# Performance work log

Hardware: AMD Instinct MI355X
Metric: run time of the kernel (lower is better)

Reference implementation:

```python
import jax, jax.numpy as jnp
import numpy as np

LAMDA = 1.0


def setup_inputs() -> dict:
    key = jax.random.key(0)
    k1, k2, k3, k4 = jax.random.split(key, 4)
    B, C, D = 16384, 1000, 512
    logits = jax.random.normal(k1, (B, C), dtype=jnp.float32)
    labels = jax.random.randint(k2, (B,), 0, C, dtype=jnp.int64)
    features = jax.random.normal(k3, (B, D), dtype=jnp.float32)
    global_protos = jax.random.normal(k4, (C, D), dtype=jnp.float32)
    return {"logits": logits, "labels": labels, "features": features,
            "global_protos": global_protos}


def reference(logits, labels, features, global_protos):
    # --- classification loss: mean cross-entropy ---
    logp = jax.nn.log_softmax(logits, axis=-1)                 # [B, C]
    ce_loss = -jnp.take_along_axis(logp, labels[:, None], axis=1).mean()
    ce_loss = jnp.where(jnp.isfinite(ce_loss), ce_loss, 0.0)

    # --- prototype alignment loss ---
    # Every label has a (finite) global prototype, so the per-sample dict
    # loop reduces to: gather proto by label, per-sample MSE, mean over B.
    gathered = global_protos[labels]                           # [B, D]
    per_sample_mse = jnp.mean((features - gathered) ** 2, axis=-1)  # [B]
    proto_loss = per_sample_mse.mean()

    total_loss = ce_loss + LAMDA * proto_loss
    total_loss = jnp.where(jnp.isfinite(total_loss), total_loss, ce_loss)
    return (total_loss, ce_loss, proto_loss)
```

## Files before the change

kernel.cpp:

```cpp
#include <hip/hip_runtime.h>
#include <math.h>


#ifndef INFINITY
#define INFINITY __builtin_inff()
#endif

#define NB_MAX 2048

__global__ __launch_bounds__(256) void fedtgp_rows(
    const float* __restrict__ logits,
    const int*   __restrict__ labels,
    const float* __restrict__ features,
    const float* __restrict__ protos,
    double* __restrict__ ce_part,
    double* __restrict__ pl_part,
    int B, int C, int D)
{
    const int tid  = threadIdx.x;
    const int lane = tid & 63;
    const int wv   = tid >> 6;

    __shared__ float rmax[4];
    __shared__ float rsum[4];
    __shared__ float rsq[4];

    const int C4 = C >> 2;
    const int D4 = D >> 2;

    double ce_acc = 0.0;
    double pl_acc = 0.0;

    for (int row = blockIdx.x; row < B; row += gridDim.x) {
        const int lab = labels[row];
        const float4* lrow4 = (const float4*)(logits + (size_t)row * C);

        float4 lv = make_float4(0.f, 0.f, 0.f, 0.f);
        float m = -INFINITY;
        if (tid < C4) {
            lv = lrow4[tid];
            m = fmaxf(fmaxf(lv.x, lv.y), fmaxf(lv.z, lv.w));
        }
        #pragma unroll
        for (int off = 32; off > 0; off >>= 1)
            m = fmaxf(m, __shfl_xor(m, off, 64));
        if (lane == 0) rmax[wv] = m;
        __syncthreads();
        const float bmax = fmaxf(fmaxf(rmax[0], rmax[1]), fmaxf(rmax[2], rmax[3]));

        float s = 0.f;
        if (tid < C4) {
            s = __expf(lv.x - bmax) + __expf(lv.y - bmax)
              + __expf(lv.z - bmax) + __expf(lv.w - bmax);
        }
        #pragma unroll
        for (int off = 32; off > 0; off >>= 1)
            s += __shfl_xor(s, off, 64);
        if (lane == 0) rsum[wv] = s;

        float q = 0.f;
        if (tid < D4) {
            const float4 f = ((const float4*)(features + (size_t)row * D))[tid];
            const float4 p = ((const float4*)(protos   + (size_t)lab * D))[tid];
            const float dx = f.x - p.x, dy = f.y - p.y;
            const float dz = f.z - p.z, dw = f.w - p.w;
            q = dx*dx + dy*dy + dz*dz + dw*dw;
        }
        #pragma unroll
        for (int off = 32; off > 0; off >>= 1)
            q += __shfl_xor(q, off, 64);
        if (lane == 0) rsq[wv] = q;
        __syncthreads();

        if (tid == 0) {
            const float bsum = rsum[0] + rsum[1] + rsum[2] + rsum[3];
            const float bsq  = rsq[0]  + rsq[1]  + rsq[2]  + rsq[3];
            const float lse  = bmax + __logf(bsum);
            const float ce_b = lse - logits[(size_t)row * C + lab];
            ce_acc += (double)ce_b;
            pl_acc += (double)(bsq / (float)D);
        }
    }

    if (tid == 0) {
        ce_part[blockIdx.x] = ce_acc;
        pl_part[blockIdx.x] = pl_acc;
    }
}

__global__ __launch_bounds__(256) void fedtgp_finalize(
    const double* __restrict__ ce_part,
    const double* __restrict__ pl_part,
    float* __restrict__ out,
    int npart, double invB)
{
    const int tid  = threadIdx.x;
    const int lane = tid & 63;
    const int wv   = tid >> 6;
    __shared__ double rc[4];
    __shared__ double rp[4];

    double c = 0.0, p = 0.0;
    for (int i = tid; i < npart; i += 256) {
        c += ce_part[i];
        p += pl_part[i];
    }
    #pragma unroll
    for (int off = 32; off > 0; off >>= 1) {
        c += __shfl_xor(c, off, 64);
        p += __shfl_xor(p, off, 64);
    }
    if (lane == 0) { rc[wv] = c; rp[wv] = p; }
    __syncthreads();

    if (tid == 0) {
        const double cs = rc[0] + rc[1] + rc[2] + rc[3];
        const double ps = rp[0] + rp[1] + rp[2] + rp[3];
        float ce = (float)(cs * invB);
        float pl = (float)(ps * invB);
        if (!isfinite(ce)) ce = 0.0f;
        float tot = ce + pl;
        if (!isfinite(tot)) tot = ce;
        out[0] = tot;
        out[1] = ce;
        out[2] = pl;
    }
}

extern "C" void kernel_launch(void* const* d_in, const int* in_sizes, int n_in,
                              void* d_out, int out_size, void* d_ws, size_t ws_size,
                              hipStream_t stream)
{
    const float* logits   = (const float*)d_in[0];
    const int*   labels   = (const int*)  d_in[1];
    const float* features = (const float*)d_in[2];
    const float* protos   = (const float*)d_in[3];
    float* out = (float*)d_out;

    const int B = in_sizes[1];
    const int C = in_sizes[0] / B;
    const int D = in_sizes[2] / B;

    int nb = NB_MAX;
    const size_t need_per_block = 2 * sizeof(double);
    if ((size_t)nb * need_per_block > ws_size) {
        nb = (int)(ws_size / need_per_block);
        if (nb < 1) nb = 1;
    }
    if (nb > B) nb = B;

    double* ce_part = (double*)d_ws;
    double* pl_part = ce_part + nb;

    fedtgp_rows<<<nb, 256, 0, stream>>>(logits, labels, features, protos,
                                        ce_part, pl_part, B, C, D);
    fedtgp_finalize<<<1, 256, 0, stream>>>(ce_part, pl_part, out, nb, 1.0 / (double)B);
}
```

Before: 124.3 us.

## Process one row per wavefront with online softmax and shuffle-only reductions

Each row is now handled by a single 64-lane wavefront rather than a 256-thread block. Each lane computes an online max/sum-exp over strided float4 chunks, and the per-lane partials are merged with a shuffle butterfly. This removes the two __syncthreads and the shared-memory round trips per row, and also handles C or D values that are not multiples of 4. In exchange each wave issues more serial loads per row with fewer lanes active (250 float4 per 64 lanes), and the clamp of nb to B was removed.

New measurement: 121.6 us. -2.2%, faster.

```diff
diff --git a/kernel.cpp b/kernel.cpp
--- a/kernel.cpp
+++ b/kernel.cpp
@@ -6,7 +6,7 @@
 #define INFINITY __builtin_inff()
 #endif
 
-#define NB_MAX 2048
+#define NB 2048
 
 __global__ __launch_bounds__(256) void fedtgp_rows(
     const float* __restrict__ logits,
@@ -20,71 +20,91 @@
     const int tid  = threadIdx.x;
     const int lane = tid & 63;
     const int wv   = tid >> 6;
+    const int gw     = blockIdx.x * 4 + wv;
+    const int nwaves = gridDim.x * 4;
 
-    __shared__ float rmax[4];
-    __shared__ float rsum[4];
-    __shared__ float rsq[4];
+    const int C4   = C >> 2;
+    const int Crem = C & 3;
+    const int D4   = D >> 2;
+    const int Drem = D & 3;
 
-    const int C4 = C >> 2;
-    const int D4 = D >> 2;
+    double ce_acc = 0.0, pl_acc = 0.0;
 
-    double ce_acc = 0.0;
-    double pl_acc = 0.0;
+    for (int row = gw; row < B; row += nwaves) {
+        const float*  lrow = logits + (size_t)row * C;
+        const float4* l4   = (const float4*)lrow;
+        const int lab = labels[row];
+        const float ll = lrow[lab];
 
-    for (int row = blockIdx.x; row < B; row += gridDim.x) {
-        const int lab = labels[row];
-        const float4* lrow4 = (const float4*)(logits + (size_t)row * C);
+        float m = -INFINITY, s = 0.f;
+        for (int base = 0; base < C4; base += 256) {
+            float4 v[4];
+            #pragma unroll
+            for (int k = 0; k < 4; ++k) {
+                const int idx = base + lane + 64 * k;
+                v[k] = (idx < C4) ? l4[idx]
+                                  : make_float4(-INFINITY, -INFINITY, -INFINITY, -INFINITY);
+            }
+            float cm = m;
+            #pragma unroll
+            for (int k = 0; k < 4; ++k)
+                cm = fmaxf(cm, fmaxf(fmaxf(v[k].x, v[k].y), fmaxf(v[k].z, v[k].w)));
+            if (cm > -INFINITY) {
+                s *= __expf(m - cm);
+                #pragma unroll
+                for (int k = 0; k < 4; ++k) {
+                    s += __expf(v[k].x - cm) + __expf(v[k].y - cm)
+                       + __expf(v[k].z - cm) + __expf(v[k].w - cm);
+                }
+                m = cm;
+            }
+        }
+        if (Crem && lane < Crem) {
+            const float x = lrow[(C4 << 2) + lane];
+            const float cm = fmaxf(m, x);
+            s = s * __expf(m - cm) + __expf(x - cm);
+            m = cm;
+        }
 
-        float4 lv = make_float4(0.f, 0.f, 0.f, 0.f);
-        float m = -INFINITY;
-        if (tid < C4) {
-            lv = lrow4[tid];
-            m = fmaxf(fmaxf(lv.x, lv.y), fmaxf(lv.z, lv.w));
-        }
-        #pragma unroll
-        for (int off = 32; off > 0; off >>= 1)
-            m = fmaxf(m, __shfl_xor(m, off, 64));
-        if (lane == 0) rmax[wv] = m;
-        __syncthreads();
-        const float bmax = fmaxf(fmaxf(rmax[0], rmax[1]), fmaxf(rmax[2], rmax[3]));
-
-        float s = 0.f;
-        if (tid < C4) {
-            s = __expf(lv.x - bmax) + __expf(lv.y - bmax)
-              + __expf(lv.z - bmax) + __expf(lv.w - bmax);
-        }
-        #pragma unroll
-        for (int off = 32; off > 0; off >>= 1)
-            s += __shfl_xor(s, off, 64);
-        if (lane == 0) rsum[wv] = s;
-
+        const float4* f4 = (const float4*)(features + (size_t)row * D);
+        const float4* p4 = (const float4*)(protos   + (size_t)lab * D);
         float q = 0.f;
-        if (tid < D4) {
-            const float4 f = ((const float4*)(features + (size_t)row * D))[tid];
-            const float4 p = ((const float4*)(protos   + (size_t)lab * D))[tid];
+        for (int idx = lane; idx < D4; idx += 64) {
+            const float4 f = f4[idx];
+            const float4 p = p4[idx];
             const float dx = f.x - p.x, dy = f.y - p.y;
             const float dz = f.z - p.z, dw = f.w - p.w;
-            q = dx*dx + dy*dy + dz*dz + dw*dw;
+            q += dx * dx + dy * dy + dz * dz + dw * dw;
         }
+        if (Drem && lane < Drem) {
+            const float df = features[(size_t)row * D + (D4 << 2) + lane]
+                           - protos[(size_t)lab * D + (D4 << 2) + lane];
+            q += df * df;
+        }
+
         #pragma unroll
-        for (int off = 32; off > 0; off >>= 1)
+        for (int off = 32; off > 0; off >>= 1) {
+            const float om = __shfl_xor(m, off, 64);
+            const float os = __shfl_xor(s, off, 64);
+            const float nm = fmaxf(m, om);
+            s = s * __expf(m - nm) + os * __expf(om - nm);
+            m = nm;
             q += __shfl_xor(q, off, 64);
-        if (lane == 0) rsq[wv] = q;
-        __syncthreads();
+        }
 
-        if (tid == 0) {
-            const float bsum = rsum[0] + rsum[1] + rsum[2] + rsum[3];
-            const float bsq  = rsq[0]  + rsq[1]  + rsq[2]  + rsq[3];
-            const float lse  = bmax + __logf(bsum);
-            const float ce_b = lse - logits[(size_t)row * C + lab];
-            ce_acc += (double)ce_b;
-            pl_acc += (double)(bsq / (float)D);
+        if (lane == 0) {
+            const float lse = m + __logf(s);
+            ce_acc += (double)(lse - ll);
+            pl_acc += (double)(q / (float)D);
         }
     }
 
+    __shared__ double sc[4], sp[4];
+    if (lane == 0) { sc[wv] = ce_acc; sp[wv] = pl_acc; }
+    __syncthreads();
     if (tid == 0) {
-        ce_part[blockIdx.x] = ce_acc;
-        pl_part[blockIdx.x] = pl_acc;
+        ce_part[blockIdx.x] = sc[0] + sc[1] + sc[2] + sc[3];
+        pl_part[blockIdx.x] = sp[0] + sp[1] + sp[2] + sp[3];
     }
 }
 
@@ -141,13 +161,12 @@
     const int C = in_sizes[0] / B;
     const int D = in_sizes[2] / B;
 
-    int nb = NB_MAX;
+    int nb = NB;
     const size_t need_per_block = 2 * sizeof(double);
     if ((size_t)nb * need_per_block > ws_size) {
         nb = (int)(ws_size / need_per_block);
         if (nb < 1) nb = 1;
     }
-    if (nb > B) nb = B;
 
     double* ce_part = (double*)d_ws;
     double* pl_part = ce_part + nb;
```
